# Kernel optimization log

Measured on AMD Instinct MI355X. Metric: run time of the kernel, lower is better.

## Reference

```python
import jax, jax.numpy as jnp
import numpy as np

B, T, D, H, O = 8, 16384, 256, 256, 256


def setup_inputs() -> dict:
    key = jax.random.key(0)
    ks = jax.random.split(key, 7)
    lim_d = 1.0 / np.sqrt(D)
    lim_h = 1.0 / np.sqrt(H)
    u = lambda k, shape, lim: jax.random.uniform(k, shape, jnp.float32, -lim, lim)
    return {
        "xs": jax.random.normal(ks[0], (B, T, D), jnp.float32),
        "Wz": u(ks[1], (H, D), lim_d),
        "bz": u(ks[2], (H,), lim_d),
        "Wh": u(ks[3], (H, D), lim_d),
        "bh": u(ks[4], (H,), lim_d),
        "Wo": u(ks[5], (O, H), lim_h),
        "bo": u(ks[6], (O,), lim_h),
    }


def reference(xs, Wz, bz, Wh, bh, Wo, bo):
    # gates and candidate hidden states (eqx.nn.Linear: y = W @ x + b)
    zs = jax.nn.sigmoid(jnp.einsum("btd,hd->bth", xs, Wz) + bz)  # [B,T,H]
    hs = jnp.einsum("btd,hd->bth", xs, Wh) + bh                  # [B,T,H]

    # prepend_ones / prepend_zeros along the time axis
    a = jnp.concatenate([jnp.ones_like(zs[:, :1]), 1.0 - zs], axis=1)    # [B,T+1,H]
    b = jnp.concatenate([jnp.zeros_like(zs[:, :1]), zs * hs], axis=1)    # [B,T+1,H]

    def combine(first, second):
        a0, b0 = first
        a1, b1 = second
        return (a0 * b0, b0 * a1 + b1)

    _, states = jax.lax.associative_scan(combine, (a, b), axis=1)
    return jnp.einsum("bth,oh->bto", states[:, 1:], Wo) + bo  # [B,T,O]
```

## Files before the change

kernel.cpp:

```cpp
#include <hip/hip_runtime.h>

#define Bsz 8
#define Tsz 16384
#define NL0 16385
#define NL5 512
#define NL10 16

typedef __attribute__((ext_vector_type(2))) float f32x2;
typedef __attribute__((ext_vector_type(4))) float f32x4;
typedef __attribute__((ext_vector_type(8))) short bf16x8;

__device__ __forceinline__ short f2bf(float f) {
  unsigned u = __builtin_bit_cast(unsigned, f);
  u += 0x7FFFu + ((u >> 16) & 1u);
  return (short)(u >> 16);
}
__device__ __forceinline__ bf16x8 pack8(f32x4 a, f32x4 b) {
  bf16x8 v;
  v[0] = f2bf(a[0]); v[1] = f2bf(a[1]); v[2] = f2bf(a[2]); v[3] = f2bf(a[3]);
  v[4] = f2bf(b[0]); v[5] = f2bf(b[1]); v[6] = f2bf(b[2]); v[7] = f2bf(b[3]);
  return v;
}
__device__ __forceinline__ void unpk(unsigned u, float& a, float& b) {
  a = __builtin_bit_cast(float, u << 16);
  b = __builtin_bit_cast(float, u & 0xFFFF0000u);
}

__global__ void fill_sentinel(float* __restrict__ out, int n) {
  int i = blockIdx.x * blockDim.x + threadIdx.x;
  if (i < n) out[i] = 12345.0f;
}

__global__ void prep_weights(const float* __restrict__ Wz, const float* __restrict__ Wh,
                             const float* __restrict__ Wo, unsigned short* __restrict__ wt) {
  int idx = blockIdx.x * 256 + threadIdx.x;
  if (idx >= 3 * 256 * 32) return;
  int m   = idx >> 13;
  int rem = idx & 8191;
  int r   = rem >> 5;
  int cq  = rem & 31;
  const float* src = (m == 0 ? Wz : (m == 1 ? Wh : Wo)) + r * 256 + cq * 8;
  f32x4 v0 = *(const f32x4*)src;
  f32x4 v1 = *(const f32x4*)(src + 4);
  *(bf16x8*)(wt + m * 65536 + (cq * 256 + r) * 8) = pack8(v0, v1);
}

__global__ void init_e0(unsigned* __restrict__ l0) {
  int idx = blockIdx.x * 256 + threadIdx.x;
  if (idx >= Bsz * 256) return;
  int batch = idx >> 8, h = idx & 255;
  l0[(size_t)batch * NL0 * 256 + h] = 0x00003F80u;
}

__global__ __launch_bounds__(512, 4)
void gemm_zh(const float* __restrict__ xs, const unsigned short* __restrict__ wt,
             const float* __restrict__ bz, const float* __restrict__ bh,
             unsigned* __restrict__ l0)
{
  __shared__ __align__(16) unsigned short aL[2][4096];

  const int tid = threadIdx.x;
  const int wave = tid >> 6, lane = tid & 63, l15 = lane & 15, l4 = lane >> 4;
  const int rowBase = blockIdx.x * 64;
  const int srow = tid & 63, soct = tid >> 6;
  const float* aptr = xs + (size_t)(rowBase + srow) * 256 + soct * 8;
  const unsigned short* wz_t = wt;
  const unsigned short* wh_t = wt + 65536;

  f32x4 accz[4][2] = {};
  f32x4 acch[4][2] = {};

  f32x4 av0 = *(const f32x4*)(aptr);
  f32x4 av1 = *(const f32x4*)(aptr + 4);
  *(bf16x8*)&aL[0][(soct * 64 + srow) * 8] = pack8(av0, av1);

  const int wn = wave * 32;
  for (int S = 0; S < 4; ++S) {
    __syncthreads();
    const int cur = S & 1;
    if (S < 3) {
      av0 = *(const f32x4*)(aptr + (S + 1) * 64);
      av1 = *(const f32x4*)(aptr + (S + 1) * 64 + 4);
    }
#pragma unroll
    for (int k2 = 0; k2 < 2; ++k2) {
      bf16x8 af[4], zf[2], hf[2];
#pragma unroll
      for (int m = 0; m < 4; ++m)
        af[m] = *(const bf16x8*)&aL[cur][((k2 * 4 + l4) * 64 + m * 16 + l15) * 8];
      const int cq = (S * 2 + k2) * 4 + l4;
#pragma unroll
      for (int n = 0; n < 2; ++n) {
        const int r = wn + n * 16 + l15;
        zf[n] = *(const bf16x8*)(wz_t + (cq * 256 + r) * 8);
        hf[n] = *(const bf16x8*)(wh_t + (cq * 256 + r) * 8);
      }
#pragma unroll
      for (int m = 0; m < 4; ++m)
#pragma unroll
        for (int n = 0; n < 2; ++n) {
          accz[m][n] = __builtin_amdgcn_mfma_f32_16x16x32_bf16(af[m], zf[n], accz[m][n], 0, 0, 0);
          acch[m][n] = __builtin_amdgcn_mfma_f32_16x16x32_bf16(af[m], hf[n], acch[m][n], 0, 0, 0);
        }
    }
    if (S < 3)
      *(bf16x8*)&aL[cur ^ 1][(soct * 64 + srow) * 8] = pack8(av0, av1);
  }

  const int batch = rowBase >> 14;
  const int tRow  = rowBase & (Tsz - 1);
#pragma unroll
  for (int n = 0; n < 2; ++n) {
    const int col = wn + n * 16 + l15;
    const float bzv = bz[col], bhv = bh[col];
#pragma unroll
    for (int m = 0; m < 4; ++m)
#pragma unroll
      for (int j = 0; j < 4; ++j) {
        const int t = tRow + m * 16 + l4 * 4 + j;
        const float zv = 1.0f / (1.0f + __expf(-(accz[m][n][j] + bzv)));
        const float hv = acch[m][n][j] + bhv;
        unsigned u = (unsigned)(unsigned short)f2bf(1.0f - zv)
                   | ((unsigned)(unsigned short)f2bf(zv * hv) << 16);
        l0[((size_t)batch * NL0 + t + 1) * 256 + col] = u;
      }
  }
}

__global__ __launch_bounds__(256)
void chunk_up_bf16(const unsigned* __restrict__ l0, f32x2* __restrict__ dst)
{
  int idx = blockIdx.x * 256 + threadIdx.x;
  int h2 = idx & 127, r = idx >> 7;
  int c = r & 511, batch = r >> 9;
  size_t base = ((size_t)batch * NL0 + (size_t)c * 32) * 256 + h2 * 2;

  float ax[16], bx[16], ay[16], by[16];
#pragma unroll
  for (int i = 0; i < 16; ++i) {
    uint2 e0 = *(const uint2*)(l0 + base + (size_t)(2 * i) * 256);
    uint2 e1 = *(const uint2*)(l0 + base + (size_t)(2 * i + 1) * 256);
    float a0, b0, a1, b1;
    unpk(e0.x, a0, b0); unpk(e1.x, a1, b1);
    ax[i] = a0 * b0; bx[i] = b0 * a1 + b1;
    unpk(e0.y, a0, b0); unpk(e1.y, a1, b1);
    ay[i] = a0 * b0; by[i] = b0 * a1 + b1;
  }
#pragma unroll
  for (int n = 8; n >= 1; n >>= 1) {
#pragma unroll
    for (int i = 0; i < n; ++i) {
      float nax = ax[2*i] * bx[2*i], nbx = bx[2*i] * ax[2*i+1] + bx[2*i+1];
      float nay = ay[2*i] * by[2*i], nby = by[2*i] * ay[2*i+1] + by[2*i+1];
      ax[i] = nax; bx[i] = nbx; ay[i] = nay; by[i] = nby;
    }
  }
  f32x4 o = {ax[0], bx[0], ay[0], by[0]};
  *(f32x4*)((float*)dst + (((size_t)batch * 512 + c) * 256 + h2 * 2) * 2) = o;
}

__global__ __launch_bounds__(256)
void chunk_up(const f32x2* __restrict__ src, f32x2* __restrict__ dst, int nCh, int nSrc)
{
  int idx = blockIdx.x * 256 + threadIdx.x;
  int total = Bsz * nCh * 256;
  if (idx >= total) return;
  int h = idx & 255, r = idx >> 8;
  int c = r % nCh, batch = r / nCh;
  size_t base = ((size_t)batch * nSrc + (size_t)c * 32) * 256 + h;

  float a1[16], b1[16];
#pragma unroll
  for (int i = 0; i < 16; ++i) {
    f32x2 e0 = src[base + (size_t)(2 * i) * 256];
    f32x2 e1 = src[base + (size_t)(2 * i + 1) * 256];
    a1[i] = e0[0] * e0[1];
    b1[i] = e0[1] * e1[0] + e1[1];
  }
#pragma unroll
  for (int n = 8; n >= 1; n >>= 1) {
#pragma unroll
    for (int i = 0; i < n; ++i) {
      float na = a1[2 * i] * b1[2 * i];
      float nb = b1[2 * i] * a1[2 * i + 1] + b1[2 * i + 1];
      a1[i] = na; b1[i] = nb;
    }
  }
  dst[((size_t)batch * nCh + c) * 256 + h] = f32x2{a1[0], b1[0]};
}

__global__ void tree16(const f32x2* __restrict__ src, float* __restrict__ outB)
{
  int idx = blockIdx.x * 256 + threadIdx.x;
  if (idx >= Bsz * 256) return;
  int h = idx & 255, batch = idx >> 8;
  size_t base = (size_t)batch * 16 * 256 + h;

  float a0[16], b0[16];
#pragma unroll
  for (int i = 0; i < 16; ++i) { f32x2 e = src[base + (size_t)i * 256]; a0[i] = e[0]; b0[i] = e[1]; }
  float a1[8], b1[8];
#pragma unroll
  for (int i = 0; i < 8; ++i) { a1[i] = a0[2*i]*b0[2*i]; b1[i] = b0[2*i]*a0[2*i+1] + b0[2*i+1]; }
  float a2[4], b2[4];
#pragma unroll
  for (int i = 0; i < 4; ++i) { a2[i] = a1[2*i]*b1[2*i]; b2[i] = b1[2*i]*a1[2*i+1] + b1[2*i+1]; }
  float a3[2], b3[2];
#pragma unroll
  for (int i = 0; i < 2; ++i) { a3[i] = a2[2*i]*b2[2*i]; b3[i] = b2[2*i]*a2[2*i+1] + b2[2*i+1]; }
  float s3[2];
  s3[0] = b3[0];
  s3[1] = b3[0] * a3[1] + b3[1];
  float s2[4];
  s2[0] = b2[0]; s2[1] = s3[0]; s2[2] = s3[0] * a2[2] + b2[2]; s2[3] = s3[1];
  float s1[8];
  s1[0] = b1[0];
#pragma unroll
  for (int j = 0; j < 4; ++j) s1[2*j+1] = s2[j];
#pragma unroll
  for (int j = 1; j < 4; ++j) s1[2*j] = s2[j-1] * a1[2*j] + b1[2*j];
  float s0[16];
  s0[0] = b0[0];
#pragma unroll
  for (int j = 0; j < 8; ++j) s0[2*j+1] = s1[j];
#pragma unroll
  for (int j = 1; j < 8; ++j) s0[2*j] = s1[j-1] * a0[2*j] + b0[2*j];
#pragma unroll
  for (int i = 0; i < 16; ++i) outB[base + (size_t)i * 256] = s0[i];
}

__global__ __launch_bounds__(256, 2)
void chunk_down_f32(const f32x2* __restrict__ src, const float* __restrict__ snext,
                    float* __restrict__ outF, int nCh, int nFull, int nSrc)
{
  int idx = blockIdx.x * 256 + threadIdx.x;
  int total = Bsz * nCh * 256;
  if (idx >= total) return;
  int h = idx & 255, r = idx >> 8;
  int c = r % nCh, batch = r / nCh;
  size_t base = ((size_t)batch * nSrc + (size_t)c * 32) * 256 + h;
  bool hasP = (c > 0);
  float P = hasP ? snext[((size_t)batch * nFull + (c - 1)) * 256 + h] : 0.0f;
  float S = snext[((size_t)batch * nFull + c) * 256 + h];

  float ae[16], be[16], a1[16], b1[16];
#pragma unroll
  for (int i = 0; i < 16; ++i) {
    f32x2 e0 = src[base + (size_t)(2 * i) * 256];
    f32x2 e1 = src[base + (size_t)(2 * i + 1) * 256];
    ae[i] = e0[0]; be[i] = e0[1];
    a1[i] = e0[0] * e0[1];
    b1[i] = e0[1] * e1[0] + e1[1];
  }
  float a2[8], b2[8];
#pragma unroll
  for (int i = 0; i < 8; ++i) { a2[i] = a1[2*i]*b1[2*i]; b2[i] = b1[2*i]*a1[2*i+1] + b1[2*i+1]; }
  float a3[4], b3[4];
#pragma unroll
  for (int i = 0; i < 4; ++i) { a3[i] = a2[2*i]*b2[2*i]; b3[i] = b2[2*i]*a2[2*i+1] + b2[2*i+1]; }
  float a4[2], b4[2];
#pragma unroll
  for (int i = 0; i < 2; ++i) { a4[i] = a3[2*i]*b3[2*i]; b4[i] = b3[2*i]*a3[2*i+1] + b3[2*i+1]; }

  float s4[2];
  s4[0] = hasP ? P * a4[0] + b4[0] : b4[0];
  s4[1] = S;
  float s3[4];
  s3[0] = hasP ? P * a3[0] + b3[0] : b3[0];
  s3[1] = s4[0]; s3[2] = s4[0] * a3[2] + b3[2]; s3[3] = s4[1];
  float s2[8];
  s2[0] = hasP ? P * a2[0] + b2[0] : b2[0];
#pragma unroll
  for (int j = 0; j < 4; ++j) s2[2*j+1] = s3[j];
#pragma unroll
  for (int j = 1; j < 4; ++j) s2[2*j] = s3[j-1] * a2[2*j] + b2[2*j];
  float s1[16];
  s1[0] = hasP ? P * a1[0] + b1[0] : b1[0];
#pragma unroll
  for (int j = 0; j < 8; ++j) s1[2*j+1] = s2[j];
#pragma unroll
  for (int j = 1; j < 8; ++j) s1[2*j] = s2[j-1] * a1[2*j] + b1[2*j];

  outF[base] = hasP ? P * ae[0] + be[0] : be[0];
#pragma unroll
  for (int j = 0; j < 16; ++j) outF[base + (size_t)(2*j+1) * 256] = s1[j];
#pragma unroll
  for (int j = 1; j < 16; ++j) outF[base + (size_t)(2*j) * 256] = s1[j-1] * ae[j] + be[j];
}

__global__ __launch_bounds__(256, 2)
void down_proj(const unsigned* __restrict__ l0, const float* __restrict__ s5b,
               const unsigned short* __restrict__ wo_t, const float* __restrict__ bo,
               float* __restrict__ out)
{
  __shared__ unsigned short pL[32 * 256];

  const int tid = threadIdx.x;
  const int bc = blockIdx.x;
  const int c = bc % 513;
  const int batch = bc / 513;

  {
    const int h = tid;
    const size_t base = ((size_t)batch * NL0 + (size_t)c * 32) * 256 + h;
    const bool hasP = (c > 0);
    const float P = hasP ? s5b[((size_t)batch * 512 + (c - 1)) * 256 + h] : 0.0f;

    if (c == 512) {
      float a0, b0; unpk(l0[base], a0, b0);
      pL[h] = (unsigned short)f2bf(P * a0 + b0);
#pragma unroll
      for (int i = 1; i < 32; ++i)
        pL[i * 256 + (h ^ ((i & 7) << 3))] = 0;
    } else {
      const float S = s5b[((size_t)batch * 512 + c) * 256 + h];
      float ae[16], be[16], a1[16], b1[16];
#pragma unroll
      for (int i = 0; i < 16; ++i) {
        unsigned u0 = l0[base + (size_t)(2 * i) * 256];
        unsigned u1 = l0[base + (size_t)(2 * i + 1) * 256];
        float a0, b0, a1e, b1e;
        unpk(u0, a0, b0); unpk(u1, a1e, b1e);
        ae[i] = a0; be[i] = b0;
        a1[i] = a0 * b0; b1[i] = b0 * a1e + b1e;
      }
      float a2[8], b2[8];
#pragma unroll
      for (int i = 0; i < 8; ++i) { a2[i] = a1[2*i]*b1[2*i]; b2[i] = b1[2*i]*a1[2*i+1] + b1[2*i+1]; }
      float a3[4], b3[4];
#pragma unroll
      for (int i = 0; i < 4; ++i) { a3[i] = a2[2*i]*b2[2*i]; b3[i] = b2[2*i]*a2[2*i+1] + b2[2*i+1]; }
      float a4[2], b4[2];
#pragma unroll
      for (int i = 0; i < 2; ++i) { a4[i] = a3[2*i]*b3[2*i]; b4[i] = b3[2*i]*a3[2*i+1] + b3[2*i+1]; }

      float s4[2];
      s4[0] = hasP ? P * a4[0] + b4[0] : b4[0];
      s4[1] = S;
      float s3[4];
      s3[0] = hasP ? P * a3[0] + b3[0] : b3[0];
      s3[1] = s4[0]; s3[2] = s4[0] * a3[2] + b3[2]; s3[3] = s4[1];
      float s2[8];
      s2[0] = hasP ? P * a2[0] + b2[0] : b2[0];
#pragma unroll
      for (int j = 0; j < 4; ++j) s2[2*j+1] = s3[j];
#pragma unroll
      for (int j = 1; j < 4; ++j) s2[2*j] = s3[j-1] * a2[2*j] + b2[2*j];
      float s1[16];
      s1[0] = hasP ? P * a1[0] + b1[0] : b1[0];
#pragma unroll
      for (int j = 0; j < 8; ++j) s1[2*j+1] = s2[j];
#pragma unroll
      for (int j = 1; j < 8; ++j) s1[2*j] = s2[j-1] * a1[2*j] + b1[2*j];

      pL[h] = (unsigned short)f2bf(hasP ? P * ae[0] + be[0] : be[0]);
#pragma unroll
      for (int j = 0; j < 16; ++j) {
        const int row = 2 * j + 1;
        pL[row * 256 + (h ^ ((row & 7) << 3))] = (unsigned short)f2bf(s1[j]);
      }
#pragma unroll
      for (int j = 1; j < 16; ++j) {
        const int row = 2 * j;
        pL[row * 256 + (h ^ ((row & 7) << 3))] = (unsigned short)f2bf(s1[j-1] * ae[j] + be[j]);
      }
    }
  }
  __syncthreads();

  const int wave = tid >> 6, lane = tid & 63, l15 = lane & 15, l4 = lane >> 4;
  const int wn = wave * 64;
  f32x4 acc[2][4] = {};
#pragma unroll
  for (int kk = 0; kk < 8; ++kk) {
    bf16x8 af[2], wf[4];
#pragma unroll
    for (int m = 0; m < 2; ++m) {
      const int row = m * 16 + l15;
      af[m] = *(const bf16x8*)&pL[row * 256 + ((kk * 32 + l4 * 8) ^ ((row & 7) << 3))];
    }
#pragma unroll
    for (int n = 0; n < 4; ++n)
      wf[n] = *(const bf16x8*)(wo_t + ((kk * 4 + l4) * 256 + wn + n * 16 + l15) * 8);
#pragma unroll
    for (int m = 0; m < 2; ++m)
#pragma unroll
      for (int n = 0; n < 4; ++n)
        acc[m][n] = __builtin_amdgcn_mfma_f32_16x16x32_bf16(af[m], wf[n], acc[m][n], 0, 0, 0);
  }

  const int tBase = 32 * c - 1;
#pragma unroll
  for (int n = 0; n < 4; ++n) {
    const int col = wn + n * 16 + l15;
    const float bv = bo[col];
#pragma unroll
    for (int m = 0; m < 2; ++m)
#pragma unroll
      for (int j = 0; j < 4; ++j) {
        const int t = tBase + m * 16 + l4 * 4 + j;
        if ((unsigned)t < (unsigned)Tsz)
          out[((size_t)batch * Tsz + t) * 256 + col] = acc[m][n][j] + bv;
      }
  }
}

extern "C" void kernel_launch(void* const* d_in, const int* in_sizes, int n_in,
                              void* d_out, int out_size, void* d_ws, size_t ws_size,
                              hipStream_t stream)
{
  (void)in_sizes; (void)n_in;
  const float* xs = (const float*)d_in[0];
  const float* Wz = (const float*)d_in[1];
  const float* bz = (const float*)d_in[2];
  const float* Wh = (const float*)d_in[3];
  const float* bh = (const float*)d_in[4];
  const float* Wo = (const float*)d_in[5];
  const float* bo = (const float*)d_in[6];
  float* out = (float*)d_out;

  const size_t n_l0  = (size_t)Bsz * NL0 * 256;
  const size_t n_l5  = (size_t)Bsz * NL5 * 256;
  const size_t n_l10 = (size_t)Bsz * NL10 * 256;

  unsigned* l0    = (unsigned*)d_ws;
  f32x2* l5ab     = (f32x2*)(l0 + n_l0);
  f32x2* l10ab    = l5ab + n_l5;
  float* s10b     = (float*)(l10ab + n_l10);
  float* s5b      = s10b + n_l10;
  unsigned short* wt = (unsigned short*)(s5b + n_l5);

  const size_t need = n_l0 * 4 + n_l5 * 8 + n_l10 * 8 + n_l10 * 4 + n_l5 * 4 + 3 * 65536 * 2;
  if (ws_size < need) {
    fill_sentinel<<<(out_size + 255) / 256, 256, 0, stream>>>(out, out_size);
    return;
  }

  prep_weights<<<96, 256, 0, stream>>>(Wz, Wh, Wo, wt);
  init_e0<<<8, 256, 0, stream>>>(l0);
  gemm_zh<<<Bsz * Tsz / 64, 512, 0, stream>>>(xs, wt, bz, bh, l0);

  chunk_up_bf16<<<(Bsz * 512 * 128) / 256, 256, 0, stream>>>(l0, l5ab);
  chunk_up<<<(Bsz * 16 * 256) / 256, 256, 0, stream>>>(l5ab, l10ab, 16, NL5);
  tree16<<<8, 256, 0, stream>>>(l10ab, s10b);
  chunk_down_f32<<<(Bsz * 16 * 256) / 256, 256, 0, stream>>>(l5ab, s10b, s5b, 16, 16, NL5);

  down_proj<<<Bsz * 513, 256, 0, stream>>>(l0, s5b, wt + 2 * 65536, bo, out);
}
```

Before: 183.2 us.

## Prefetch weight fragments, use packed bf16 converts and nontemporal memory ops

The gate/candidate GEMM and the down-projection now register-double-buffer their B-operand (weight) fragments, loading step k+1 while issuing MFMAs for step k. Scalar bf16 rounding is replaced by the packed float2-to-bfloat162 conversion intrinsic. Streaming loads of xs and the intermediate buffer, and stores of the output, use nontemporal hints. The gemm_zh occupancy hint drops from 4 to 3 blocks so the extra prefetch registers fit, which lowers the number of resident waves.

```diff
diff --git a/kernel.cpp b/kernel.cpp
--- a/kernel.cpp
+++ b/kernel.cpp
@@ -1,4 +1,5 @@
 #include <hip/hip_runtime.h>
+#include <hip/hip_bf16.h>
 
 #define Bsz 8
 #define Tsz 16384
@@ -15,11 +16,17 @@
   u += 0x7FFFu + ((u >> 16) & 1u);
   return (short)(u >> 16);
 }
+__device__ __forceinline__ unsigned cvtpk(float lo, float hi) {
+  __hip_bfloat162 t = __float22bfloat162_rn(float2{lo, hi});
+  unsigned u;
+  __builtin_memcpy(&u, &t, 4);
+  return u;
+}
 __device__ __forceinline__ bf16x8 pack8(f32x4 a, f32x4 b) {
-  bf16x8 v;
-  v[0] = f2bf(a[0]); v[1] = f2bf(a[1]); v[2] = f2bf(a[2]); v[3] = f2bf(a[3]);
-  v[4] = f2bf(b[0]); v[5] = f2bf(b[1]); v[6] = f2bf(b[2]); v[7] = f2bf(b[3]);
-  return v;
+  union { unsigned u[4]; bf16x8 v; } r;
+  r.u[0] = cvtpk(a[0], a[1]); r.u[1] = cvtpk(a[2], a[3]);
+  r.u[2] = cvtpk(b[0], b[1]); r.u[3] = cvtpk(b[2], b[3]);
+  return r.v;
 }
 __device__ __forceinline__ void unpk(unsigned u, float& a, float& b) {
   a = __builtin_bit_cast(float, u << 16);
@@ -52,7 +59,7 @@
   l0[(size_t)batch * NL0 * 256 + h] = 0x00003F80u;
 }
 
-__global__ __launch_bounds__(512, 4)
+__global__ __launch_bounds__(512, 3)
 void gemm_zh(const float* __restrict__ xs, const unsigned short* __restrict__ wt,
              const float* __restrict__ bz, const float* __restrict__ bh,
              unsigned* __restrict__ l0)
@@ -66,45 +73,59 @@
   const float* aptr = xs + (size_t)(rowBase + srow) * 256 + soct * 8;
   const unsigned short* wz_t = wt;
   const unsigned short* wh_t = wt + 65536;
+  const int wn = wave * 32;
 
   f32x4 accz[4][2] = {};
   f32x4 acch[4][2] = {};
 
-  f32x4 av0 = *(const f32x4*)(aptr);
-  f32x4 av1 = *(const f32x4*)(aptr + 4);
+  f32x4 av0 = __builtin_nontemporal_load((const f32x4*)aptr);
+  f32x4 av1 = __builtin_nontemporal_load((const f32x4*)(aptr + 4));
   *(bf16x8*)&aL[0][(soct * 64 + srow) * 8] = pack8(av0, av1);
 
-  const int wn = wave * 32;
-  for (int S = 0; S < 4; ++S) {
-    __syncthreads();
-    const int cur = S & 1;
-    if (S < 3) {
-      av0 = *(const f32x4*)(aptr + (S + 1) * 64);
-      av1 = *(const f32x4*)(aptr + (S + 1) * 64 + 4);
-    }
-#pragma unroll
-    for (int k2 = 0; k2 < 2; ++k2) {
-      bf16x8 af[4], zf[2], hf[2];
-#pragma unroll
-      for (int m = 0; m < 4; ++m)
-        af[m] = *(const bf16x8*)&aL[cur][((k2 * 4 + l4) * 64 + m * 16 + l15) * 8];
-      const int cq = (S * 2 + k2) * 4 + l4;
+  bf16x8 zc[2], hc[2], zn[2], hn[2];
+#pragma unroll
+  for (int n = 0; n < 2; ++n) {
+    const int r = wn + n * 16 + l15;
+    zc[n] = *(const bf16x8*)(wz_t + (l4 * 256 + r) * 8);
+    hc[n] = *(const bf16x8*)(wh_t + (l4 * 256 + r) * 8);
+  }
+
+#pragma unroll
+  for (int kk = 0; kk < 8; ++kk) {
+    const int S = kk >> 1;
+    if ((kk & 1) == 0) {
+      __syncthreads();
+      if (S < 3) {
+        av0 = __builtin_nontemporal_load((const f32x4*)(aptr + (S + 1) * 64));
+        av1 = __builtin_nontemporal_load((const f32x4*)(aptr + (S + 1) * 64 + 4));
+      }
+    }
+    if (kk < 7) {
+      const int cq = (kk + 1) * 4 + l4;
 #pragma unroll
       for (int n = 0; n < 2; ++n) {
         const int r = wn + n * 16 + l15;
-        zf[n] = *(const bf16x8*)(wz_t + (cq * 256 + r) * 8);
-        hf[n] = *(const bf16x8*)(wh_t + (cq * 256 + r) * 8);
-      }
-#pragma unroll
-      for (int m = 0; m < 4; ++m)
-#pragma unroll
-        for (int n = 0; n < 2; ++n) {
-          accz[m][n] = __builtin_amdgcn_mfma_f32_16x16x32_bf16(af[m], zf[n], accz[m][n], 0, 0, 0);
-          acch[m][n] = __builtin_amdgcn_mfma_f32_16x16x32_bf16(af[m], hf[n], acch[m][n], 0, 0, 0);
-        }
-    }
-    if (S < 3)
-      *(bf16x8*)&aL[cur ^ 1][(soct * 64 + srow) * 8] = pack8(av0, av1);
+        zn[n] = *(const bf16x8*)(wz_t + (cq * 256 + r) * 8);
+        hn[n] = *(const bf16x8*)(wh_t + (cq * 256 + r) * 8);
+      }
+    }
+    bf16x8 af[4];
+#pragma unroll
+    for (int m = 0; m < 4; ++m)
+      af[m] = *(const bf16x8*)&aL[S & 1][(((kk & 1) * 4 + l4) * 64 + m * 16 + l15) * 8];
+#pragma unroll
+    for (int m = 0; m < 4; ++m)
+#pragma unroll
+      for (int n = 0; n < 2; ++n) {
+        accz[m][n] = __builtin_amdgcn_mfma_f32_16x16x32_bf16(af[m], zc[n], accz[m][n], 0, 0, 0);
+        acch[m][n] = __builtin_amdgcn_mfma_f32_16x16x32_bf16(af[m], hc[n], acch[m][n], 0, 0, 0);
+      }
+    if ((kk & 1) && S < 3)
+      *(bf16x8*)&aL[(S & 1) ^ 1][(soct * 64 + srow) * 8] = pack8(av0, av1);
+    if (kk < 7) {
+      zc[0] = zn[0]; zc[1] = zn[1];
+      hc[0] = hn[0]; hc[1] = hn[1];
+    }
   }
 
   const int batch = rowBase >> 14;
@@ -120,9 +141,7 @@
         const int t = tRow + m * 16 + l4 * 4 + j;
         const float zv = 1.0f / (1.0f + __expf(-(accz[m][n][j] + bzv)));
         const float hv = acch[m][n][j] + bhv;
-        unsigned u = (unsigned)(unsigned short)f2bf(1.0f - zv)
-                   | ((unsigned)(unsigned short)f2bf(zv * hv) << 16);
-        l0[((size_t)batch * NL0 + t + 1) * 256 + col] = u;
+        l0[((size_t)batch * NL0 + t + 1) * 256 + col] = cvtpk(1.0f - zv, zv * hv);
       }
   }
 }
@@ -307,7 +326,7 @@
     const float P = hasP ? s5b[((size_t)batch * 512 + (c - 1)) * 256 + h] : 0.0f;
 
     if (c == 512) {
-      float a0, b0; unpk(l0[base], a0, b0);
+      float a0, b0; unpk(__builtin_nontemporal_load(l0 + base), a0, b0);
       pL[h] = (unsigned short)f2bf(P * a0 + b0);
 #pragma unroll
       for (int i = 1; i < 32; ++i)
@@ -317,8 +336,8 @@
       float ae[16], be[16], a1[16], b1[16];
 #pragma unroll
       for (int i = 0; i < 16; ++i) {
-        unsigned u0 = l0[base + (size_t)(2 * i) * 256];
-        unsigned u1 = l0[base + (size_t)(2 * i + 1) * 256];
+        unsigned u0 = __builtin_nontemporal_load(l0 + base + (size_t)(2 * i) * 256);
+        unsigned u1 = __builtin_nontemporal_load(l0 + base + (size_t)(2 * i + 1) * 256);
         float a0, b0, a1e, b1e;
         unpk(u0, a0, b0); unpk(u1, a1e, b1e);
         ae[i] = a0; be[i] = b0;
@@ -371,22 +390,31 @@
   const int wave = tid >> 6, lane = tid & 63, l15 = lane & 15, l4 = lane >> 4;
   const int wn = wave * 64;
   f32x4 acc[2][4] = {};
+  bf16x8 wc[4], wnx[4];
+#pragma unroll
+  for (int n = 0; n < 4; ++n)
+    wc[n] = *(const bf16x8*)(wo_t + (l4 * 256 + wn + n * 16 + l15) * 8);
 #pragma unroll
   for (int kk = 0; kk < 8; ++kk) {
-    bf16x8 af[2], wf[4];
+    if (kk < 7) {
+#pragma unroll
+      for (int n = 0; n < 4; ++n)
+        wnx[n] = *(const bf16x8*)(wo_t + (((kk + 1) * 4 + l4) * 256 + wn + n * 16 + l15) * 8);
+    }
+    bf16x8 af[2];
 #pragma unroll
     for (int m = 0; m < 2; ++m) {
       const int row = m * 16 + l15;
       af[m] = *(const bf16x8*)&pL[row * 256 + ((kk * 32 + l4 * 8) ^ ((row & 7) << 3))];
     }
 #pragma unroll
-    for (int n = 0; n < 4; ++n)
-      wf[n] = *(const bf16x8*)(wo_t + ((kk * 4 + l4) * 256 + wn + n * 16 + l15) * 8);
-#pragma unroll
     for (int m = 0; m < 2; ++m)
 #pragma unroll
       for (int n = 0; n < 4; ++n)
-        acc[m][n] = __builtin_amdgcn_mfma_f32_16x16x32_bf16(af[m], wf[n], acc[m][n], 0, 0, 0);
+        acc[m][n] = __builtin_amdgcn_mfma_f32_16x16x32_bf16(af[m], wc[n], acc[m][n], 0, 0, 0);
+    if (kk < 7) {
+      wc[0] = wnx[0]; wc[1] = wnx[1]; wc[2] = wnx[2]; wc[3] = wnx[3];
+    }
   }
 
   const int tBase = 32 * c - 1;
@@ -400,7 +428,8 @@
       for (int j = 0; j < 4; ++j) {
         const int t = tBase + m * 16 + l4 * 4 + j;
         if ((unsigned)t < (unsigned)Tsz)
-          out[((size_t)batch * Tsz + t) * 256 + col] = acc[m][n][j] + bv;
+          __builtin_nontemporal_store(acc[m][n][j] + bv,
+                                      &out[((size_t)batch * Tsz + t) * 256 + col]);
       }
   }
 }
```

Measured after the change: 199.7 us. 1.09x slower.
